# Optimization experiments

Measured on AMD Instinct MI355X. Metric: run time of the kernel, lower is better.

## Reference

```python
import jax, jax.numpy as jnp
import numpy as np

N_NODES = 100000
N_EDGES = 1600000
IN_F = 128
OUT_F = 64


def setup_inputs() -> dict:
    key = jax.random.key(0)
    ks = jax.random.split(key, 9)
    x = jax.random.normal(ks[0], (N_NODES, IN_F), dtype=jnp.float32)
    Wv = jax.random.normal(ks[1], (IN_F, OUT_F), dtype=jnp.float32) / np.sqrt(IN_F)
    bv = jax.random.normal(ks[2], (OUT_F,), dtype=jnp.float32) * 0.02
    wq = jax.random.normal(ks[3], (OUT_F,), dtype=jnp.float32) / np.sqrt(OUT_F)
    bq = jax.random.normal(ks[4], (1,), dtype=jnp.float32) * 0.02
    wk = jax.random.normal(ks[5], (OUT_F,), dtype=jnp.float32) / np.sqrt(OUT_F)
    bk = jax.random.normal(ks[6], (1,), dtype=jnp.float32) * 0.02
    src = jax.random.randint(ks[7], (N_EDGES,), 0, N_NODES, dtype=jnp.int64)
    dst = jax.random.randint(ks[8], (N_EDGES,), 0, N_NODES, dtype=jnp.int64)
    return {"x": x, "Wv": Wv, "bv": bv, "wq": wq, "bq": bq,
            "wk": wk, "bk": bk, "src": src, "dst": dst}


def reference(x, Wv, bv, wq, bq, wk, bk, src, dst):
    n = x.shape[0]
    # node transform (linear_v) and scalar scores (linear_q, linear_k)
    xv = x @ Wv + bv                      # [N, OUT_F]
    el = xv @ wq + bq[0]                  # [N] source score
    er = xv @ wk + bk[0]                  # [N] destination score
    # per-edge score: u_add_v + leaky_relu(0.2)
    e = jax.nn.leaky_relu(el[src] + er[dst], negative_slope=0.2)  # [E]
    # edge softmax over incoming edges of each dst (numerically stable)
    emax = jax.ops.segment_max(e, dst, num_segments=n)            # [N]
    ex = jnp.exp(e - emax[dst])                                   # [E]
    denom = jax.ops.segment_sum(ex, dst, num_segments=n)          # [N]
    attn = ex / denom[dst]                                        # [E]
    # u_mul_e + aggregate_sum: weighted scatter of source features into dst
    out = jax.ops.segment_sum(xv[src] * attn[:, None], dst, num_segments=n)
    return out
```

## Files before the change

### kernel.cpp

```cpp
#include <hip/hip_runtime.h>
#include <hip/hip_bf16.h>

#define NN 100000
#define NE 1600000
#define IN_F 128
#define OUT_F 64
#define NBINS 196
#define BIN_SHIFT 9
#define GEMM_WGS 1563
#define P1_WGS 391
#define NREP2 8
#define SUBCAP 1280

typedef __attribute__((ext_vector_type(8))) short bf16x8;
typedef __attribute__((ext_vector_type(4))) float f32x4;

__device__ __forceinline__ short f2bf(float f) {
  unsigned u = __float_as_uint(f);
  unsigned r = (u + 0x7fffu + ((u >> 16) & 1u)) >> 16;
  return (short)r;
}
__device__ __forceinline__ float bf2f(ushort u) {
  return __uint_as_float(((unsigned)u) << 16);
}

__global__ __launch_bounds__(256) void prep_w(
    const float* __restrict__ Wv, short* __restrict__ wvt) {
  const int i = blockIdx.x * 256 + threadIdx.x;
  if (i >= IN_F * OUT_F) return;
  const int j = i >> 7, k = i & 127;
  wvt[i] = f2bf(Wv[k * OUT_F + j]);
}

__global__ __launch_bounds__(256) void fused_tp(
    const float* __restrict__ x, const short* __restrict__ wvt,
    const float* __restrict__ bv, const float* __restrict__ wq,
    const float* __restrict__ bq, const float* __restrict__ wk,
    const float* __restrict__ bk,
    ushort* __restrict__ xvb, float* __restrict__ el, float* __restrict__ er,
    const int* __restrict__ src, const int* __restrict__ dst,
    int* __restrict__ bincur, unsigned* __restrict__ slab) {
  if (blockIdx.x >= GEMM_WGS) {
    __shared__ int hist[NBINS];
    __shared__ int base_[NBINS];
    const int pb = blockIdx.x - GEMM_WGS;
    const int t = threadIdx.x;
    const int rep = pb & (NREP2 - 1);
    for (int i = t; i < NBINS; i += 256) hist[i] = 0;
    __syncthreads();
    const int e0 = pb * 4096;
    int sv[16], dv[16];
#pragma unroll
    for (int r = 0; r < 16; ++r) {
      const int i = e0 + r * 256 + t;
      if (i < NE) {
        sv[r] = src[i];
        dv[r] = dst[i];
        atomicAdd(&hist[dv[r] >> BIN_SHIFT], 1);
      } else {
        sv[r] = -1;
        dv[r] = 0;
      }
    }
    __syncthreads();
    for (int b = t; b < NBINS; b += 256) {
      base_[b] = (hist[b] > 0) ? atomicAdd(&bincur[rep * NBINS + b], hist[b]) : 0;
      hist[b] = 0;
    }
    __syncthreads();
#pragma unroll
    for (int r = 0; r < 16; ++r) {
      if (sv[r] >= 0) {
        const int s = sv[r], d = dv[r];
        const int b = d >> BIN_SHIFT;
        const unsigned dl = (unsigned)(d & 511);
        const int pos = base_[b] + atomicAdd(&hist[b], 1);
        slab[(size_t)(b * NREP2 + rep) * SUBCAP + pos] = (dl << 17) | (unsigned)s;
      }
    }
    return;
  }

  const int wave = threadIdx.x >> 6, lane = threadIdx.x & 63;
  const int node0 = blockIdx.x * 64 + wave * 16;
  const int j15 = lane & 15, g = lane >> 4;
  const int kb = g * 8;

  int row = node0 + j15;
  if (row >= NN) row = NN - 1;
  const float* xr = x + (size_t)row * IN_F;
  bf16x8 a[4];
#pragma unroll
  for (int kt = 0; kt < 4; ++kt) {
    const float4 f0 = *(const float4*)(xr + kt * 32 + kb);
    const float4 f1 = *(const float4*)(xr + kt * 32 + kb + 4);
    bf16x8 t;
    t[0] = f2bf(f0.x); t[1] = f2bf(f0.y); t[2] = f2bf(f0.z); t[3] = f2bf(f0.w);
    t[4] = f2bf(f1.x); t[5] = f2bf(f1.y); t[6] = f2bf(f1.z); t[7] = f2bf(f1.w);
    a[kt] = t;
  }

  bf16x8 b[16];
#pragma unroll
  for (int nt = 0; nt < 4; ++nt)
#pragma unroll
    for (int kt = 0; kt < 4; ++kt)
      b[nt * 4 + kt] = *(const bf16x8*)(wvt + (size_t)(nt * 16 + j15) * IN_F + kt * 32 + kb);

  f32x4 acc[4];
#pragma unroll
  for (int nt = 0; nt < 4; ++nt) acc[nt] = (f32x4){0.f, 0.f, 0.f, 0.f};
#pragma unroll
  for (int nt = 0; nt < 4; ++nt)
#pragma unroll
    for (int kt = 0; kt < 4; ++kt)
      acc[nt] = __builtin_amdgcn_mfma_f32_16x16x32_bf16(a[kt], b[nt * 4 + kt], acc[nt], 0, 0, 0);

  float bvl[4], wql[4], wkl[4];
#pragma unroll
  for (int nt = 0; nt < 4; ++nt) {
    bvl[nt] = bv[nt * 16 + j15];
    wql[nt] = wq[nt * 16 + j15];
    wkl[nt] = wk[nt * 16 + j15];
  }
  const float bq0 = bq[0], bk0 = bk[0];

#pragma unroll
  for (int r = 0; r < 4; ++r) {
    const int node = node0 + g * 4 + r;
    float pq = 0.f, pk = 0.f;
#pragma unroll
    for (int nt = 0; nt < 4; ++nt) {
      const float v = acc[nt][r] + bvl[nt];
      if (node < NN) xvb[(size_t)node * OUT_F + nt * 16 + j15] = (ushort)f2bf(v);
      pq += v * wql[nt];
      pk += v * wkl[nt];
    }
#pragma unroll
    for (int o = 1; o < 16; o <<= 1) {
      pq += __shfl_xor(pq, o);
      pk += __shfl_xor(pk, o);
    }
    if (j15 == 0 && node < NN) {
      el[node] = pq + bq0;
      er[node] = pk + bk0;
    }
  }
}

__global__ __launch_bounds__(256) void bin_scatter(
    const unsigned* __restrict__ slab, const int* __restrict__ bincur,
    const float* __restrict__ el, const float* __restrict__ er,
    int* __restrict__ off, uint2* __restrict__ csr) {
  __shared__ int cnt2[512];
  __shared__ int sp[256];
  __shared__ float er_l[512];
  const int b = blockIdx.x, t = threadIdx.x;
  const int n0 = b << BIN_SHIFT;

  int tot = 0;
  if (t < NBINS) {
#pragma unroll
    for (int r = 0; r < NREP2; ++r) tot += bincur[r * NBINS + t];
  }
  sp[t] = tot;
  __syncthreads();
  for (int o = 1; o < 256; o <<= 1) {
    const int u = (t >= o) ? sp[t - o] : 0;
    __syncthreads();
    sp[t] += u;
    __syncthreads();
  }
  const int csr0 = (b > 0) ? sp[b - 1] : 0;
  __syncthreads();

  cnt2[t] = 0; cnt2[t + 256] = 0;
  {
    const int n = n0 + t;
    er_l[t] = (n < NN) ? er[n] : 0.f;
    const int n2 = n0 + 256 + t;
    er_l[256 + t] = (n2 < NN) ? er[n2] : 0.f;
  }
  __syncthreads();

#pragma unroll
  for (int rep = 0; rep < NREP2; ++rep) {
    const int cnt = bincur[rep * NBINS + b];
    const unsigned* sl = slab + (size_t)(b * NREP2 + rep) * SUBCAP;
    for (int i = t; i < cnt; i += 256)
      atomicAdd(&cnt2[sl[i] >> 17], 1);
  }
  __syncthreads();

  const int c0 = cnt2[2 * t], c1 = cnt2[2 * t + 1];
  const int psum = c0 + c1;
  sp[t] = psum;
  __syncthreads();
  for (int o = 1; o < 256; o <<= 1) {
    const int u = (t >= o) ? sp[t - o] : 0;
    __syncthreads();
    sp[t] += u;
    __syncthreads();
  }
  const int excl = sp[t] - psum;
  const int cur0 = csr0 + excl, cur1 = csr0 + excl + c0;
  cnt2[2 * t] = cur0;
  cnt2[2 * t + 1] = cur1;
  if (n0 + 2 * t < NN) off[n0 + 2 * t] = cur0;
  if (n0 + 2 * t + 1 < NN) off[n0 + 2 * t + 1] = cur1;
  if (b == NBINS - 1 && t == 0) off[NN] = NE;
  __syncthreads();

#pragma unroll
  for (int rep = 0; rep < NREP2; ++rep) {
    const int cnt = bincur[rep * NBINS + b];
    const unsigned* sl = slab + (size_t)(b * NREP2 + rep) * SUBCAP;
    for (int i = t; i < cnt; i += 256) {
      const unsigned w = sl[i];
      const int dl = (int)(w >> 17);
      const int s = (int)(w & 0x1FFFFu);
      float e = el[s] + er_l[dl];
      e = e > 0.f ? e : 0.2f * e;
      const int pos = atomicAdd(&cnt2[dl], 1);
      csr[pos] = (uint2){(unsigned)s, __float_as_uint(e)};
    }
  }
}

__global__ __launch_bounds__(256) void node_aggregate(
    const ushort* __restrict__ xvb, const int* __restrict__ off,
    const uint2* __restrict__ csr, float* __restrict__ out) {
  const int wave = threadIdx.x >> 6, lane = threadIdx.x & 63;
  const int node = blockIdx.x * 4 + wave;
  if (node >= NN) return;
  const int base = off[node];
  const int deg = off[node + 1] - base;

  if (deg <= 64) {
    const bool valid = lane < deg;
    uint2 w = valid ? csr[base + lane] : (uint2){0u, 0u};
    int s = (int)w.x;
    float p = valid ? __expf(__uint_as_float(w.y)) : 0.f;
    float t = p;
#pragma unroll
    for (int o = 32; o; o >>= 1) t += __shfl_xor(t, o);
    p *= (deg > 0) ? (1.0f / t) : 0.f;

    const int fgrp = lane & 7, egrp = lane >> 3;
    float4 aLo = {0.f, 0.f, 0.f, 0.f};
    float4 aHi = {0.f, 0.f, 0.f, 0.f};
    const int nr = (deg + 7) >> 3;
#pragma unroll 4
    for (int r = 0; r < nr; ++r) {
      const int k = (r << 3) + egrp;
      const int sk = __shfl(s, k);
      const float pk = __shfl(p, k);
      if (k < deg) {
        const uint4 v = *(const uint4*)(xvb + (size_t)sk * OUT_F + (fgrp << 3));
        aLo.x += pk * __uint_as_float(v.x << 16);
        aLo.y += pk * __uint_as_float(v.x & 0xffff0000u);
        aLo.z += pk * __uint_as_float(v.y << 16);
        aLo.w += pk * __uint_as_float(v.y & 0xffff0000u);
        aHi.x += pk * __uint_as_float(v.z << 16);
        aHi.y += pk * __uint_as_float(v.z & 0xffff0000u);
        aHi.z += pk * __uint_as_float(v.w << 16);
        aHi.w += pk * __uint_as_float(v.w & 0xffff0000u);
      }
    }
#pragma unroll
    for (int o = 8; o <= 32; o <<= 1) {
      aLo.x += __shfl_xor(aLo.x, o);
      aLo.y += __shfl_xor(aLo.y, o);
      aLo.z += __shfl_xor(aLo.z, o);
      aLo.w += __shfl_xor(aLo.w, o);
      aHi.x += __shfl_xor(aHi.x, o);
      aHi.y += __shfl_xor(aHi.y, o);
      aHi.z += __shfl_xor(aHi.z, o);
      aHi.w += __shfl_xor(aHi.w, o);
    }
    if (egrp == 0) {
      float* op = out + (size_t)node * OUT_F + (fgrp << 3);
      *(float4*)op = aLo;
      *(float4*)(op + 4) = aHi;
    }
  } else {
    float m = -3.0e38f;
    for (int k = lane; k < deg; k += 64) m = fmaxf(m, __uint_as_float(csr[base + k].y));
#pragma unroll
    for (int o = 32; o; o >>= 1) m = fmaxf(m, __shfl_xor(m, o));
    float ssum = 0.f;
    for (int k = lane; k < deg; k += 64) ssum += __expf(__uint_as_float(csr[base + k].y) - m);
#pragma unroll
    for (int o = 32; o; o >>= 1) ssum += __shfl_xor(ssum, o);
    const float inv = 1.0f / ssum;
    float acc = 0.f;
    for (int k = 0; k < deg; ++k) {
      const uint2 w = csr[base + k];
      const float pk = __expf(__uint_as_float(w.y) - m) * inv;
      acc += pk * bf2f(xvb[(size_t)w.x * OUT_F + lane]);
    }
    out[(size_t)node * OUT_F + lane] = acc;
  }
}

extern "C" void kernel_launch(void* const* d_in, const int* in_sizes, int n_in,
                              void* d_out, int out_size, void* d_ws, size_t ws_size,
                              hipStream_t stream) {
  const float* x  = (const float*)d_in[0];
  const float* Wv = (const float*)d_in[1];
  const float* bv = (const float*)d_in[2];
  const float* wq = (const float*)d_in[3];
  const float* bq = (const float*)d_in[4];
  const float* wk = (const float*)d_in[5];
  const float* bk = (const float*)d_in[6];
  const int* src  = (const int*)d_in[7];
  const int* dst  = (const int*)d_in[8];
  float* out = (float*)d_out;

  ushort* xvb = (ushort*)d_ws;
  float* el = (float*)(xvb + (size_t)NN * OUT_F);
  float* er = el + NN;
  int* off = (int*)(er + NN);
  uint2* csr = (uint2*)(off + NN + 2);
  unsigned* slab = (unsigned*)(csr + NE);
  short* wvt = (short*)(slab + (size_t)NBINS * NREP2 * SUBCAP);
  int* bincur = (int*)(wvt + IN_F * OUT_F);

  hipMemsetAsync(bincur, 0, NREP2 * NBINS * sizeof(int), stream);

  prep_w<<<(IN_F * OUT_F + 255) / 256, 256, 0, stream>>>(Wv, wvt);
  fused_tp<<<GEMM_WGS + P1_WGS, 256, 0, stream>>>(x, wvt, bv, wq, bq, wk, bk,
                                                  xvb, el, er, src, dst, bincur, slab);
  bin_scatter<<<NBINS, 256, 0, stream>>>(slab, bincur, el, er, off, csr);
  node_aggregate<<<(NN + 3) / 4, 256, 0, stream>>>(xvb, off, csr, out);
}
```

Before: 123.6 us.

## Use finer destination bins in bin_scatter and fold bincur zeroing into prep_w

Shrinks each destination bin from 512 to 128 nodes, so bin_scatter launches 782 workgroups instead of 196 and fills more of the GPU. The inter-bin prefix scan now covers four bins per thread, with an extra per-block fix-up for the remainder. The separate hipMemsetAsync is removed and the counters are zeroed inside prep_w, saving one launch. In exchange, the per-bin slab capacity is much smaller, so a bin that overflows it would be corrupted, and the fused_tp histogram now atomics into more global counters.

```diff
diff --git a/kernel.cpp b/kernel.cpp
--- a/kernel.cpp
+++ b/kernel.cpp
@@ -5,12 +5,12 @@
 #define NE 1600000
 #define IN_F 128
 #define OUT_F 64
-#define NBINS 196
-#define BIN_SHIFT 9
+#define NBINS 782
+#define BIN_SHIFT 7
 #define GEMM_WGS 1563
 #define P1_WGS 391
 #define NREP2 8
-#define SUBCAP 1280
+#define SUBCAP 384
 
 typedef __attribute__((ext_vector_type(8))) short bf16x8;
 typedef __attribute__((ext_vector_type(4))) float f32x4;
@@ -25,7 +25,10 @@
 }
 
 __global__ __launch_bounds__(256) void prep_w(
-    const float* __restrict__ Wv, short* __restrict__ wvt) {
+    const float* __restrict__ Wv, short* __restrict__ wvt,
+    int* __restrict__ bincur) {
+  if (blockIdx.x == 0)
+    for (int i = threadIdx.x; i < NREP2 * NBINS; i += 256) bincur[i] = 0;
   const int i = blockIdx.x * 256 + threadIdx.x;
   if (i >= IN_F * OUT_F) return;
   const int j = i >> 7, k = i & 127;
@@ -73,7 +76,7 @@
       if (sv[r] >= 0) {
         const int s = sv[r], d = dv[r];
         const int b = d >> BIN_SHIFT;
-        const unsigned dl = (unsigned)(d & 511);
+        const unsigned dl = (unsigned)(d & 127);
         const int pos = base_[b] + atomicAdd(&hist[b], 1);
         slab[(size_t)(b * NREP2 + rep) * SUBCAP + pos] = (dl << 17) | (unsigned)s;
       }
@@ -152,18 +155,23 @@
     const unsigned* __restrict__ slab, const int* __restrict__ bincur,
     const float* __restrict__ el, const float* __restrict__ er,
     int* __restrict__ off, uint2* __restrict__ csr) {
-  __shared__ int cnt2[512];
   __shared__ int sp[256];
-  __shared__ float er_l[512];
+  __shared__ int cnt[128];
+  __shared__ float er_l[128];
+  __shared__ int s_csr0;
   const int b = blockIdx.x, t = threadIdx.x;
   const int n0 = b << BIN_SHIFT;
 
-  int tot = 0;
-  if (t < NBINS) {
-#pragma unroll
-    for (int r = 0; r < NREP2; ++r) tot += bincur[r * NBINS + t];
-  }
-  sp[t] = tot;
+  int v = 0;
+#pragma unroll
+  for (int j = 0; j < 4; ++j) {
+    const int bb = 4 * t + j;
+    if (bb < NBINS) {
+#pragma unroll
+      for (int r = 0; r < NREP2; ++r) v += bincur[r * NBINS + bb];
+    }
+  }
+  sp[t] = v;
   __syncthreads();
   for (int o = 1; o < 256; o <<= 1) {
     const int u = (t >= o) ? sp[t - o] : 0;
@@ -171,57 +179,58 @@
     sp[t] += u;
     __syncthreads();
   }
-  const int csr0 = (b > 0) ? sp[b - 1] : 0;
-  __syncthreads();
-
-  cnt2[t] = 0; cnt2[t + 256] = 0;
-  {
+  if (t == 0) {
+    const int q = b >> 2, rr = b & 3;
+    int c = (q > 0) ? sp[q - 1] : 0;
+    for (int j = 0; j < rr; ++j)
+      for (int r = 0; r < NREP2; ++r) c += bincur[r * NBINS + (4 * q + j)];
+    s_csr0 = c;
+  }
+  if (t < 128) {
+    cnt[t] = 0;
     const int n = n0 + t;
     er_l[t] = (n < NN) ? er[n] : 0.f;
-    const int n2 = n0 + 256 + t;
-    er_l[256 + t] = (n2 < NN) ? er[n2] : 0.f;
-  }
-  __syncthreads();
+  }
+  __syncthreads();
+  const int csr0 = s_csr0;
 
 #pragma unroll
   for (int rep = 0; rep < NREP2; ++rep) {
-    const int cnt = bincur[rep * NBINS + b];
+    const int c = bincur[rep * NBINS + b];
     const unsigned* sl = slab + (size_t)(b * NREP2 + rep) * SUBCAP;
-    for (int i = t; i < cnt; i += 256)
-      atomicAdd(&cnt2[sl[i] >> 17], 1);
-  }
-  __syncthreads();
-
-  const int c0 = cnt2[2 * t], c1 = cnt2[2 * t + 1];
-  const int psum = c0 + c1;
-  sp[t] = psum;
-  __syncthreads();
-  for (int o = 1; o < 256; o <<= 1) {
-    const int u = (t >= o) ? sp[t - o] : 0;
-    __syncthreads();
-    sp[t] += u;
-    __syncthreads();
-  }
-  const int excl = sp[t] - psum;
-  const int cur0 = csr0 + excl, cur1 = csr0 + excl + c0;
-  cnt2[2 * t] = cur0;
-  cnt2[2 * t + 1] = cur1;
-  if (n0 + 2 * t < NN) off[n0 + 2 * t] = cur0;
-  if (n0 + 2 * t + 1 < NN) off[n0 + 2 * t + 1] = cur1;
+    for (int i = t; i < c; i += 256)
+      atomicAdd(&cnt[sl[i] >> 17], 1);
+  }
+  __syncthreads();
+
+  const int cme = (t < 128) ? cnt[t] : 0;
+  sp[t] = cme;
+  __syncthreads();
+  for (int o = 1; o < 128; o <<= 1) {
+    const int u = (t >= o && t < 128) ? sp[t - o] : 0;
+    __syncthreads();
+    if (t < 128) sp[t] += u;
+    __syncthreads();
+  }
+  if (t < 128) {
+    const int cur = csr0 + sp[t] - cme;
+    cnt[t] = cur;
+    if (n0 + t < NN) off[n0 + t] = cur;
+  }
   if (b == NBINS - 1 && t == 0) off[NN] = NE;
   __syncthreads();
 
 #pragma unroll
   for (int rep = 0; rep < NREP2; ++rep) {
-    const int cnt = bincur[rep * NBINS + b];
+    const int c = bincur[rep * NBINS + b];
     const unsigned* sl = slab + (size_t)(b * NREP2 + rep) * SUBCAP;
-    for (int i = t; i < cnt; i += 256) {
+    for (int i = t; i < c; i += 256) {
       const unsigned w = sl[i];
       const int dl = (int)(w >> 17);
       const int s = (int)(w & 0x1FFFFu);
       float e = el[s] + er_l[dl];
       e = e > 0.f ? e : 0.2f * e;
-      const int pos = atomicAdd(&cnt2[dl], 1);
+      const int pos = atomicAdd(&cnt[dl], 1);
       csr[pos] = (uint2){(unsigned)s, __float_as_uint(e)};
     }
   }
@@ -326,9 +335,7 @@
   short* wvt = (short*)(slab + (size_t)NBINS * NREP2 * SUBCAP);
   int* bincur = (int*)(wvt + IN_F * OUT_F);
 
-  hipMemsetAsync(bincur, 0, NREP2 * NBINS * sizeof(int), stream);
-
-  prep_w<<<(IN_F * OUT_F + 255) / 256, 256, 0, stream>>>(Wv, wvt);
+  prep_w<<<(IN_F * OUT_F + 255) / 256, 256, 0, stream>>>(Wv, wvt, bincur);
   fused_tp<<<GEMM_WGS + P1_WGS, 256, 0, stream>>>(x, wvt, bv, wq, bq, wk, bk,
                                                   xvb, el, er, src, dst, bincur, slab);
   bin_scatter<<<NBINS, 256, 0, stream>>>(slab, bincur, el, er, off, csr);
```

New measurement: 116.5 us. 5.7% less time.
